# Performance work log

Measured on AMD Instinct MI355X. Metric: run time of the kernel, lower is better.

## Reference

```python
import jax, jax.numpy as jnp
import numpy as np

B = 50000      # batch of graphs
NOBJ = 7       # tangram pieces per graph
HID = 64
EMB = 32
SIGMA = 25.0   # VE-SDE sigma for marginal_prob_std


def _lin_init(k, fin, fout):
    kw, kb = jax.random.split(k)
    s = 1.0 / np.sqrt(fin)
    w = jax.random.uniform(kw, (fin, fout), minval=-s, maxval=s, dtype=jnp.float32)
    b = jax.random.uniform(kb, (fout,), minval=-s, maxval=s, dtype=jnp.float32)
    return w, b


def setup_inputs() -> dict:
    key = jax.random.key(0)
    ks = jax.random.split(key, 16)
    N = B * NOBJ
    omega = jax.random.normal(ks[0], (N, 3), dtype=jnp.float32)
    t = jax.random.uniform(ks[1], (B, 1), minval=1e-3, maxval=1.0, dtype=jnp.float32)
    # fully-connected edges (no self loops) per graph, offset by graph index
    a, b = np.meshgrid(np.arange(NOBJ), np.arange(NOBJ), indexing='ij')
    m = a != b
    src0, dst0 = a[m], b[m]                       # (42,)
    offs = (np.arange(B) * NOBJ)[:, None]         # (B,1)
    src = (src0[None, :] + offs).reshape(-1)
    dst = (dst0[None, :] + offs).reshape(-1)
    edge_index = jnp.asarray(np.stack([src, dst]), dtype=jnp.int32)  # (2, B*42)
    W_fourier = jax.random.normal(ks[2], (EMB // 2,), dtype=jnp.float32) * 30.0
    wi1, bi1 = _lin_init(ks[3], 3, HID)
    wi2, bi2 = _lin_init(ks[4], HID, HID)
    wt, bt = _lin_init(ks[5], EMB, EMB)
    w1a, b1a = _lin_init(ks[6], HID * 2, HID)
    w1b, b1b = _lin_init(ks[7], HID, HID)
    w2a, b2a = _lin_init(ks[8], (HID + EMB) * 2, HID)
    w2b, b2b = _lin_init(ks[9], HID, HID)
    w3a, b3a = _lin_init(ks[10], (HID + EMB) * 2, HID)
    w3b, b3b = _lin_init(ks[11], HID, 3)
    return dict(omega=omega, edge_index=edge_index, t=t, num_objs=NOBJ,
                W_fourier=W_fourier,
                wi1=wi1, bi1=bi1, wi2=wi2, bi2=bi2, wt=wt, bt=bt,
                w1a=w1a, b1a=b1a, w1b=w1b, b1b=b1b,
                w2a=w2a, b2a=b2a, w2b=w2b, b2b=b2b,
                w3a=w3a, b3a=b3a, w3b=w3b, b3b=b3b)


def _mlp(x, wa, ba, wb, bb):
    return jax.nn.relu(x @ wa + ba) @ wb + bb


def reference(omega, edge_index, t, num_objs, W_fourier,
              wi1, bi1, wi2, bi2, wt, bt,
              w1a, b1a, w1b, b1b, w2a, b2a, w2b, b2b, w3a, b3a, w3b, b3b):
    N = omega.shape[0]
    src, dst = edge_index[0], edge_index[1]

    def edge_conv(x, wa, ba, wb, bb):
        # EdgeConv: msg = mlp([x_i, x_j - x_i]); max-aggregate at target i
        xi = x[dst]
        msg = _mlp(jnp.concatenate([xi, x[src] - xi], axis=-1), wa, ba, wb, bb)
        return jax.ops.segment_max(msg, dst, num_segments=N)

    init_feature = _mlp(omega, wi1, bi1, wi2, bi2)          # (N, HID)
    # Gaussian Fourier time embedding -> ReLU -> Linear -> ReLU
    proj = t[:, 0][:, None] * W_fourier[None, :] * (2.0 * jnp.pi)   # (B, EMB/2)
    emb = jnp.concatenate([jnp.sin(proj), jnp.cos(proj)], axis=-1)  # (B, EMB)
    xs = jax.nn.relu(jax.nn.relu(emb) @ wt + bt)                    # (B, EMB)
    # torch: xs.repeat(1, num_objs, 1).view(B*num_objs, -1) == tile whole block
    x_sigma = jnp.tile(xs, (num_objs, 1))                           # (N, EMB)

    x = jax.nn.relu(edge_conv(init_feature, w1a, b1a, w1b, b1b))
    x = jnp.concatenate([x, x_sigma], axis=-1)
    x = jax.nn.relu(edge_conv(x, w2a, b2a, w2b, b2b))
    x = jnp.concatenate([x, x_sigma], axis=-1)
    x = edge_conv(x, w3a, b3a, w3b, b3b)                            # (N, 3)

    # torch: t.repeat(1, num_objs).view(B*num_objs, -1) == repeat_interleave
    t_r = jnp.repeat(t, num_objs, axis=0)                           # (N, 1)
    std = jnp.sqrt((SIGMA ** (2.0 * t_r) - 1.0) / (2.0 * jnp.log(SIGMA)))
    return x / (std + 1e-7)
```

## Files before the change

### kernel.cpp

```cpp
#include <hip/hip_runtime.h>


#define NB 50000

typedef unsigned short u16;
typedef unsigned int u32;
typedef short short8 __attribute__((ext_vector_type(8)));
typedef float f32x4 __attribute__((ext_vector_type(4)));

#define OFF_I  0
#define OFF_1A 8192
#define OFF_2A 24576
#define OFF_3A 49152
#define OFF_1B 73728
#define OFF_2B 81920
#define OFF_WT 90112
#define OFF_3B 92160

#define HSTR 144
#define HLO  2304
#define H2S  272
#define XS2S 72
#define XS2LO 1152
#define SSTR 264
#define WREG 15744

__device__ __forceinline__ float b2f(u16 u) {
    return __uint_as_float(((u32)u) << 16);
}
__device__ __forceinline__ u16 f2b(float f) {
    u32 u = __float_as_uint(f);
    u += 0x7FFFu + ((u >> 16) & 1u);
    return (u16)(u >> 16);
}
__device__ __forceinline__ void split2(float v, u16& h, u16& l) {
    u32 u = __float_as_uint(v);
    h = (u16)(u >> 16);
    float d = v - __uint_as_float(u & 0xffff0000u);
    l = f2b(d);
}
__device__ __forceinline__ u32 splitpack(float v) {
    u32 u = __float_as_uint(v);
    float d = v - __uint_as_float(u & 0xffff0000u);
    u32 r = __float_as_uint(d);
    r += 0x7FFFu + ((r >> 16) & 1u);
    return __builtin_amdgcn_perm(r, u, 0x07060302);
}
__device__ __forceinline__ float bcast(float v, int l) {
    return __uint_as_float(__builtin_amdgcn_readlane(__float_as_uint(v), l));
}

__global__ __launch_bounds__(128) void pack_kernel(
    const float* __restrict__ wi2, const float* __restrict__ w1a,
    const float* __restrict__ w2a, const float* __restrict__ w3a,
    const float* __restrict__ w1b, const float* __restrict__ w2b,
    const float* __restrict__ wt,  const float* __restrict__ w3b,
    u16* __restrict__ ws)
{
    int blk = blockIdx.x;
    int j    = blockIdx.y;
    int half = threadIdx.x >> 6;
    int lane = threadIdx.x & 63;
    float v;
    u16* dst;
    if (blk < 88) {
        const float* src; int NT, qoff, obase, frag;
        if (blk < 8)       { src = wi2; NT = 4; qoff = 0;  obase = OFF_I;  frag = blk;      }
        else if (blk < 24) { src = w1a; NT = 8; qoff = 64; obase = OFF_1A; frag = blk - 8;  }
        else if (blk < 48) { src = w2a; NT = 8; qoff = 96; obase = OFF_2A; frag = blk - 24; }
        else if (blk < 72) { src = w3a; NT = 8; qoff = 96; obase = OFF_3A; frag = blk - 48; }
        else if (blk < 80) { src = w1b; NT = 4; qoff = 0;  obase = OFF_1B; frag = blk - 72; }
        else               { src = w2b; NT = 4; qoff = 0;  obase = OFF_2B; frag = blk - 80; }
        int kt = frag / NT, nt = frag % NT;
        int k = kt * 32 + (lane >> 4) * 8 + j;
        int n = nt * 16 + (lane & 15);
        int idx = (n < 64) ? (k * 64 + n) : ((qoff + k) * 64 + (n - 64));
        v = src[idx];
        dst = ws + obase + frag * 1024 + half * 512 + lane * 8 + j;
    } else if (blk < 90) {
        int frag = blk - 88;
        int k = (lane >> 4) * 8 + j;
        int n = frag * 16 + (lane & 15);
        v = wt[k * 32 + n];
        dst = ws + OFF_WT + frag * 1024 + half * 512 + lane * 8 + j;
    } else {
        int frag = blk - 90;
        int k = frag * 32 + (lane >> 4) * 8 + j;
        int n = lane & 15;
        v = (n < 3) ? w3b[k * 3 + n] : 0.f;
        dst = ws + OFF_3B + frag * 1024 + half * 512 + lane * 8 + j;
    }
    u16 hi = f2b(v);
    *dst = (half == 0) ? hi : f2b(v - b2f(hi));
}

__device__ __forceinline__ f32x4 mfma1(short8 a, short8 b, f32x4 acc) {
    return __builtin_amdgcn_mfma_f32_16x16x32_bf16(a, b, acc, 0, 0, 0);
}
__device__ __forceinline__ f32x4 mfma3(short8 ah, short8 al, short8 bh, short8 bl, f32x4 acc) {
    acc = mfma1(ah, bh, acc);
    acc = mfma1(ah, bl, acc);
    acc = mfma1(al, bh, acc);
    return acc;
}

#define ROW(k) ((k) < 7 ? (k) : (k) + 1)

__device__ __forceinline__ void writeX64_14(char* G, int L, const float* v) {
#pragma unroll
    for (int k = 0; k < 14; ++k) {
        int r = ROW(k);
        u16 h, l;
        split2(v[k], h, l);
        *(u16*)(G + r * HSTR + L * 2) = h;
        *(u16*)(G + HLO + r * HSTR + L * 2) = l;
    }
}
template<int KT>
__device__ __forceinline__ void loadA(const char* G, const char* XS2, int L,
                                      short8* Ah, short8* Al) {
#pragma unroll
    for (int kt = 0; kt < KT; ++kt) {
        if (kt < 2) {
            Ah[kt] = *(const short8*)(G + (L & 15) * HSTR + kt * 64 + (L >> 4) * 16);
            Al[kt] = *(const short8*)(G + HLO + (L & 15) * HSTR + kt * 64 + (L >> 4) * 16);
        } else {
            Ah[kt] = *(const short8*)(XS2 + (L & 15) * XS2S + (L >> 4) * 16);
            Al[kt] = *(const short8*)(XS2 + XS2LO + (L & 15) * XS2S + (L >> 4) * 16);
        }
    }
}
template<int KT, int NT>
__device__ __forceinline__ void lin_pass(const u16* __restrict__ ws, int off, int nt0,
                                         const short8* Ah, const short8* Al,
                                         char* Sg, int L) {
#pragma unroll
    for (int ntc = 0; ntc < 4; ++ntc) {
        f32x4 a1 = {0.f, 0.f, 0.f, 0.f}, a2 = {0.f, 0.f, 0.f, 0.f};
#pragma unroll
        for (int kt = 0; kt < KT; ++kt) {
            int f = kt * NT + nt0 + ntc;
            short8 bh = *(const short8*)(ws + off + f * 1024 + L * 8);
            short8 bl = *(const short8*)(ws + off + f * 1024 + 512 + L * 8);
            a1 = mfma1(Ah[kt], bh, a1);
            a2 = mfma1(Ah[kt], bl, a2);
            a2 = mfma1(Al[kt], bh, a2);
        }
#pragma unroll
        for (int rr = 0; rr < 4; ++rr)
            *(float*)(Sg + ((L >> 4) * 4 + rr) * SSTR + ntc * 64 + (L & 15) * 4) = a1[rr] + a2[rr];
    }
}
__device__ __forceinline__ void readS14(const char* Sg, int L, float* o) {
#pragma unroll
    for (int k = 0; k < 14; ++k) o[k] = *(const float*)(Sg + ROW(k) * SSTR + L * 4);
}
__device__ __forceinline__ void stageH2(char* G, int c, const float* pp, const float* qq, int L) {
#pragma unroll
    for (int r = 0; r < 16; ++r) {
        int e = c * 16 + r;
        if (e < 84) {
            int gb = (e >= 42) ? 1 : 0;
            int el = e - gb * 42;
            int i = el / 6, jj = el - i * 6;
            int j = jj + (jj >= i);
            float hv = fmaxf(pp[gb * 7 + i] + qq[gb * 7 + j], 0.f);
            *(u32*)(G + r * H2S + L * 4) = splitpack(hv);
        }
    }
}
__device__ __forceinline__ void unpack4(const uint4& a, u32* ho, u32* lo) {
    ho[0] = __builtin_amdgcn_perm(a.y, a.x, 0x05040100);
    ho[1] = __builtin_amdgcn_perm(a.w, a.z, 0x05040100);
    lo[0] = __builtin_amdgcn_perm(a.y, a.x, 0x07060302);
    lo[1] = __builtin_amdgcn_perm(a.w, a.z, 0x07060302);
}
__device__ __forceinline__ void loadAH(const char* G, int L,
                                       short8& Ah0, short8& Ah1, short8& Al0, short8& Al1) {
    const char* base = G + (L & 15) * H2S + (L >> 4) * 32;
    uint4 a0 = *(const uint4*)(base);
    uint4 a1 = *(const uint4*)(base + 16);
    uint4 b0 = *(const uint4*)(base + 128);
    uint4 b1 = *(const uint4*)(base + 144);
    union { u32 u[4]; short8 s; } h0, h1, l0, l1;
    unpack4(a0, &h0.u[0], &l0.u[0]);
    unpack4(a1, &h0.u[2], &l0.u[2]);
    unpack4(b0, &h1.u[0], &l1.u[0]);
    unpack4(b1, &h1.u[2], &l1.u[2]);
    Ah0 = h0.s; Al0 = l0.s; Ah1 = h1.s; Al1 = l1.s;
}
__device__ __forceinline__ void maxread(const char* Sb, int cc, float* mx, int L) {
#pragma unroll
    for (int r = 0; r < 16; ++r) {
        int e = cc * 16 + r;
        if (e < 84) {
            int gb = (e >= 42) ? 1 : 0;
            int i = (e - gb * 42) / 6;
            float sv = *(const float*)(Sb + r * SSTR + L * 4);
            mx[gb * 7 + i] = fmaxf(mx[gb * 7 + i], sv);
        }
    }
}

__device__ __forceinline__ void edgeconv_pipe(const u16* __restrict__ ws, int offB,
                                              char* W, char* H1, char* Sb,
                                              const float* pp, const float* qq,
                                              float vb, int L) {
    short8 Bh[8], Bl[8];
#pragma unroll
    for (int f = 0; f < 8; ++f) {
        Bh[f] = *(const short8*)(ws + offB + f * 1024 + L * 8);
        Bl[f] = *(const short8*)(ws + offB + f * 1024 + 512 + L * 8);
    }
    float mx[14];
#pragma unroll
    for (int k = 0; k < 14; ++k) mx[k] = -3.0e38f;
    stageH2(W, 0, pp, qq, L);
    short8 Ah0, Ah1, Al0, Al1;
    loadAH(W, L, Ah0, Ah1, Al0, Al1);
#pragma unroll
    for (int c = 0; c < 6; ++c) {
        char* Hn = ((c + 1) & 1) ? H1 : W;
        if (c < 5) stageH2(Hn, c + 1, pp, qq, L);
        if (c > 0) maxread(Sb, c - 1, mx, L);
#pragma unroll
        for (int nt = 0; nt < 4; ++nt) {
            f32x4 a1 = {0.f, 0.f, 0.f, 0.f}, a2 = {0.f, 0.f, 0.f, 0.f};
            a1 = mfma1(Ah0, Bh[nt], a1);
            a2 = mfma1(Ah0, Bl[nt], a2);
            a2 = mfma1(Al0, Bh[nt], a2);
            a1 = mfma1(Ah1, Bh[4 + nt], a1);
            a2 = mfma1(Ah1, Bl[4 + nt], a2);
            a2 = mfma1(Al1, Bh[4 + nt], a2);
#pragma unroll
            for (int rr = 0; rr < 4; ++rr)
                *(float*)(Sb + ((L >> 4) * 4 + rr) * SSTR + nt * 64 + (L & 15) * 4) = a1[rr] + a2[rr];
        }
        if (c < 5) loadAH(Hn, L, Ah0, Ah1, Al0, Al1);
    }
    maxread(Sb, 5, mx, L);
    float xo[14];
#pragma unroll
    for (int k = 0; k < 14; ++k) xo[k] = fmaxf(mx[k] + vb, 0.f);
    writeX64_14(W, L, xo);
}

__global__ __launch_bounds__(128) void gnn_kernel(
    const float* __restrict__ omega, const float* __restrict__ tt, const float* __restrict__ Wf,
    const float* __restrict__ wi1, const float* __restrict__ bi1, const float* __restrict__ bi2,
    const float* __restrict__ bt,
    const float* __restrict__ b1a, const float* __restrict__ b1b,
    const float* __restrict__ b2a, const float* __restrict__ b2b,
    const float* __restrict__ b3a, const float* __restrict__ b3b,
    const u16* __restrict__ ws, float* __restrict__ out)
{
    __shared__ __align__(16) char smem[2 * WREG];
    const int L   = threadIdx.x & 63;
    const int wav = threadIdx.x >> 6;
    const int p   = blockIdx.x * 2 + wav;
    const int g0  = p * 2;
    const int base0 = g0 * 7;
    char* W   = smem + wav * WREG;
    char* XS2 = W + 4608;
    char* H1  = W + 6912;
    char* Sb  = W + 11520;

    float omv = (L < 42) ? omega[base0 * 3 + L] : 0.f;
    float vwi10 = wi1[L], vwi11 = wi1[64 + L], vwi12 = wi1[128 + L];
    float vbi1 = bi1[L];
    float h1[14];
#pragma unroll
    for (int k = 0; k < 14; ++k) {
        float a0 = bcast(omv, 3 * k), a1 = bcast(omv, 3 * k + 1), a2 = bcast(omv, 3 * k + 2);
        h1[k] = fmaxf(fmaf(a0, vwi10, fmaf(a1, vwi11, fmaf(a2, vwi12, vbi1))), 0.f);
    }

    {
        int cc = L & 31;
        float vwf = Wf[cc & 15] * 6.283185307179586f;
        int tb = base0 - (base0 / NB) * NB;
#pragma unroll
        for (int k = 0; k < 14; ++k) {
            int ti = tb + k; if (ti >= NB) ti -= NB;
            float pj = tt[ti] * vwf;
            float remb = fmaxf((cc < 16) ? __sinf(pj) : __cosf(pj), 0.f);
            u16 h, l;
            split2(remb, h, l);
            if (L < 32) *(u16*)(W + ROW(k) * HSTR + cc * 2) = h;
            else *(u16*)(W + HLO + ROW(k) * HSTR + cc * 2) = l;
        }
        short8 Eh = *(const short8*)(W + (L & 15) * HSTR + (L >> 4) * 16);
        short8 El = *(const short8*)(W + HLO + (L & 15) * HSTR + (L >> 4) * 16);
#pragma unroll
        for (int nt = 0; nt < 2; ++nt) {
            short8 bh = *(const short8*)(ws + OFF_WT + nt * 1024 + L * 8);
            short8 bl = *(const short8*)(ws + OFF_WT + nt * 1024 + 512 + L * 8);
            f32x4 acc = {0.f, 0.f, 0.f, 0.f};
            acc = mfma3(Eh, El, bh, bl, acc);
#pragma unroll
            for (int rr = 0; rr < 4; ++rr)
                *(float*)(Sb + ((L >> 4) * 4 + rr) * SSTR + nt * 64 + (L & 15) * 4) = acc[rr];
        }
        float vbt = bt[cc];
#pragma unroll
        for (int k = 0; k < 14; ++k) {
            float xv = fmaxf(*(const float*)(Sb + ROW(k) * SSTR + cc * 4) + vbt, 0.f);
            u16 h, l;
            split2(xv, h, l);
            if (L < 32) *(u16*)(XS2 + ROW(k) * XS2S + cc * 2) = h;
            else *(u16*)(XS2 + XS2LO + ROW(k) * XS2S + cc * 2) = l;
        }
    }

    short8 Ah[3], Al[3];
    float pp[14], qq[14];

    writeX64_14(W, L, h1);
    loadA<2>(W, XS2, L, Ah, Al);
    lin_pass<2, 4>(ws, OFF_I, 0, Ah, Al, Sb, L);
    {
        float xh[14];
        readS14(Sb, L, xh);
        float vbi2 = bi2[L];
#pragma unroll
        for (int k = 0; k < 14; ++k) xh[k] += vbi2;
        writeX64_14(W, L, xh);
    }

    loadA<2>(W, XS2, L, Ah, Al);
    lin_pass<2, 8>(ws, OFF_1A, 0, Ah, Al, Sb, L);
    readS14(Sb, L, pp);
    lin_pass<2, 8>(ws, OFF_1A, 4, Ah, Al, Sb, L);
    readS14(Sb, L, qq);
    float vb1a = b1a[L];
#pragma unroll
    for (int k = 0; k < 14; ++k) pp[k] = pp[k] + vb1a - qq[k];
    edgeconv_pipe(ws, OFF_1B, W, H1, Sb, pp, qq, b1b[L], L);

    loadA<3>(W, XS2, L, Ah, Al);
    lin_pass<3, 8>(ws, OFF_2A, 0, Ah, Al, Sb, L);
    readS14(Sb, L, pp);
    lin_pass<3, 8>(ws, OFF_2A, 4, Ah, Al, Sb, L);
    readS14(Sb, L, qq);
    float vb2a = b2a[L];
#pragma unroll
    for (int k = 0; k < 14; ++k) pp[k] = pp[k] + vb2a - qq[k];
    edgeconv_pipe(ws, OFF_2B, W, H1, Sb, pp, qq, b2b[L], L);

    loadA<3>(W, XS2, L, Ah, Al);
    lin_pass<3, 8>(ws, OFF_3A, 0, Ah, Al, Sb, L);
    readS14(Sb, L, pp);
    lin_pass<3, 8>(ws, OFF_3A, 4, Ah, Al, Sb, L);
    readS14(Sb, L, qq);
    float vb3a = b3a[L];
#pragma unroll
    for (int k = 0; k < 14; ++k) pp[k] = pp[k] + vb3a - qq[k];

    {
        short8 B0h = *(const short8*)(ws + OFF_3B + L * 8);
        short8 B0l = *(const short8*)(ws + OFF_3B + 512 + L * 8);
        short8 B1h = *(const short8*)(ws + OFF_3B + 1024 + L * 8);
        short8 B1l = *(const short8*)(ws + OFF_3B + 1536 + L * 8);
        stageH2(W, 0, pp, qq, L);
        short8 Ah0, Ah1, Al0, Al1;
        loadAH(W, L, Ah0, Ah1, Al0, Al1);
#pragma unroll
        for (int c = 0; c < 6; ++c) {
            char* Hn = ((c + 1) & 1) ? H1 : W;
            if (c < 5) stageH2(Hn, c + 1, pp, qq, L);
            f32x4 a1 = {0.f, 0.f, 0.f, 0.f}, a2 = {0.f, 0.f, 0.f, 0.f};
            a1 = mfma1(Ah0, B0h, a1);
            a2 = mfma1(Ah0, B0l, a2);
            a2 = mfma1(Al0, B0h, a2);
            a1 = mfma1(Ah1, B1h, a1);
            a2 = mfma1(Ah1, B1l, a2);
            a2 = mfma1(Al1, B1h, a2);
            if ((L & 15) < 3) {
#pragma unroll
                for (int rr = 0; rr < 4; ++rr)
                    *(float*)(Sb + (c * 16 + (L >> 4) * 4 + rr) * 16 + (L & 15) * 4) = a1[rr] + a2[rr];
            }
            if (c < 5) loadAH(Hn, L, Ah0, Ah1, Al0, Al1);
        }
        if (L < 42) {
            int gb = (L >= 21) ? 1 : 0;
            int ll = L - gb * 21;
            int i = ll / 3, col = ll - i * 3;
            int e0 = gb * 42 + i * 6;
            float m = -3.0e38f;
#pragma unroll
            for (int e6 = 0; e6 < 6; ++e6)
                m = fmaxf(m, *(const float*)(Sb + (e0 + e6) * 16 + col * 4));
            m += b3b[col];
            float tg = tt[g0 + gb];
            float stdv = sqrtf((exp2f(tg * 9.287712379549448f) - 1.0f) * 0.15533740282828987f);
            out[base0 * 3 + L] = m / (stdv + 1e-7f);
        }
    }
}

extern "C" void kernel_launch(void* const* d_in, const int* in_sizes, int n_in,
                              void* d_out, int out_size, void* d_ws, size_t ws_size,
                              hipStream_t stream) {
    const float* omega = (const float*)d_in[0];
    const float* tt  = (const float*)d_in[2];
    const float* Wf  = (const float*)d_in[4];
    const float* wi1 = (const float*)d_in[5];
    const float* bi1 = (const float*)d_in[6];
    const float* wi2 = (const float*)d_in[7];
    const float* bi2 = (const float*)d_in[8];
    const float* wt  = (const float*)d_in[9];
    const float* bt  = (const float*)d_in[10];
    const float* w1a = (const float*)d_in[11];
    const float* b1a = (const float*)d_in[12];
    const float* w1b = (const float*)d_in[13];
    const float* b1b = (const float*)d_in[14];
    const float* w2a = (const float*)d_in[15];
    const float* b2a = (const float*)d_in[16];
    const float* w2b = (const float*)d_in[17];
    const float* b2b = (const float*)d_in[18];
    const float* w3a = (const float*)d_in[19];
    const float* b3a = (const float*)d_in[20];
    const float* w3b = (const float*)d_in[21];
    const float* b3b = (const float*)d_in[22];
    u16* ws = (u16*)d_ws;

    pack_kernel<<<dim3(92, 8), dim3(128), 0, stream>>>(wi2, w1a, w2a, w3a, w1b, w2b, wt, w3b, ws);
    gnn_kernel<<<dim3(12500), dim3(128), 0, stream>>>(
        omega, tt, Wf, wi1, bi1, bi2, bt,
        b1a, b1b, b2a, b2b, b3a, b3b, ws, (float*)d_out);
}
```

Baseline: 416.1 us.

## Shrink per-wave LDS by keeping time-embedding fragments in registers, single-buffer H

Removes the separate XS2 shared-memory region: the time-embedding A fragments are loaded once into registers (Ah2/Al2) and reused for the layer-2 and layer-3 linear passes. The H1 double buffer for edge staging is dropped, so staging writes go straight into W. Per-wave LDS falls from 15744 to 8832 bytes, and launch_bounds asks for 4 blocks per SM, both aimed at higher occupancy. The cost is extra live registers, and a single staging buffer means stageH2 for the next chunk overwrites W while the previous loadAH may still be reading it. Within one wave, program order should make that safe.

```diff
diff --git a/kernel.cpp b/kernel.cpp
--- a/kernel.cpp
+++ b/kernel.cpp
@@ -20,10 +20,8 @@
 #define HSTR 144
 #define HLO  2304
 #define H2S  272
-#define XS2S 72
-#define XS2LO 1152
 #define SSTR 264
-#define WREG 15744
+#define WREG 8832
 
 __device__ __forceinline__ float b2f(u16 u) {
     return __uint_as_float(((u32)u) << 16);
@@ -116,18 +114,11 @@
         *(u16*)(G + HLO + r * HSTR + L * 2) = l;
     }
 }
-template<int KT>
-__device__ __forceinline__ void loadA(const char* G, const char* XS2, int L,
-                                      short8* Ah, short8* Al) {
-#pragma unroll
-    for (int kt = 0; kt < KT; ++kt) {
-        if (kt < 2) {
-            Ah[kt] = *(const short8*)(G + (L & 15) * HSTR + kt * 64 + (L >> 4) * 16);
-            Al[kt] = *(const short8*)(G + HLO + (L & 15) * HSTR + kt * 64 + (L >> 4) * 16);
-        } else {
-            Ah[kt] = *(const short8*)(XS2 + (L & 15) * XS2S + (L >> 4) * 16);
-            Al[kt] = *(const short8*)(XS2 + XS2LO + (L & 15) * XS2S + (L >> 4) * 16);
-        }
+__device__ __forceinline__ void loadA2(const char* G, int L, short8* Ah, short8* Al) {
+#pragma unroll
+    for (int kt = 0; kt < 2; ++kt) {
+        Ah[kt] = *(const short8*)(G + (L & 15) * HSTR + kt * 64 + (L >> 4) * 16);
+        Al[kt] = *(const short8*)(G + HLO + (L & 15) * HSTR + kt * 64 + (L >> 4) * 16);
     }
 }
 template<int KT, int NT>
@@ -203,7 +194,7 @@
 }
 
 __device__ __forceinline__ void edgeconv_pipe(const u16* __restrict__ ws, int offB,
-                                              char* W, char* H1, char* Sb,
+                                              char* W, char* Sb,
                                               const float* pp, const float* qq,
                                               float vb, int L) {
     short8 Bh[8], Bl[8];
@@ -220,8 +211,7 @@
     loadAH(W, L, Ah0, Ah1, Al0, Al1);
 #pragma unroll
     for (int c = 0; c < 6; ++c) {
-        char* Hn = ((c + 1) & 1) ? H1 : W;
-        if (c < 5) stageH2(Hn, c + 1, pp, qq, L);
+        if (c < 5) stageH2(W, c + 1, pp, qq, L);
         if (c > 0) maxread(Sb, c - 1, mx, L);
 #pragma unroll
         for (int nt = 0; nt < 4; ++nt) {
@@ -236,7 +226,7 @@
             for (int rr = 0; rr < 4; ++rr)
                 *(float*)(Sb + ((L >> 4) * 4 + rr) * SSTR + nt * 64 + (L & 15) * 4) = a1[rr] + a2[rr];
         }
-        if (c < 5) loadAH(Hn, L, Ah0, Ah1, Al0, Al1);
+        if (c < 5) loadAH(W, L, Ah0, Ah1, Al0, Al1);
     }
     maxread(Sb, 5, mx, L);
     float xo[14];
@@ -245,7 +235,7 @@
     writeX64_14(W, L, xo);
 }
 
-__global__ __launch_bounds__(128) void gnn_kernel(
+__global__ __launch_bounds__(128, 4) void gnn_kernel(
     const float* __restrict__ omega, const float* __restrict__ tt, const float* __restrict__ Wf,
     const float* __restrict__ wi1, const float* __restrict__ bi1, const float* __restrict__ bi2,
     const float* __restrict__ bt,
@@ -261,9 +251,7 @@
     const int g0  = p * 2;
     const int base0 = g0 * 7;
     char* W   = smem + wav * WREG;
-    char* XS2 = W + 4608;
-    char* H1  = W + 6912;
-    char* Sb  = W + 11520;
+    char* Sb  = W + 4608;
 
     float omv = (L < 42) ? omega[base0 * 3 + L] : 0.f;
     float vwi10 = wi1[L], vwi11 = wi1[64 + L], vwi12 = wi1[128 + L];
@@ -275,6 +263,7 @@
         h1[k] = fmaxf(fmaf(a0, vwi10, fmaf(a1, vwi11, fmaf(a2, vwi12, vbi1))), 0.f);
     }
 
+    short8 Ah2, Al2;
     {
         int cc = L & 31;
         float vwf = Wf[cc & 15] * 6.283185307179586f;
@@ -307,16 +296,18 @@
             float xv = fmaxf(*(const float*)(Sb + ROW(k) * SSTR + cc * 4) + vbt, 0.f);
             u16 h, l;
             split2(xv, h, l);
-            if (L < 32) *(u16*)(XS2 + ROW(k) * XS2S + cc * 2) = h;
-            else *(u16*)(XS2 + XS2LO + ROW(k) * XS2S + cc * 2) = l;
-        }
+            if (L < 32) *(u16*)(W + ROW(k) * HSTR + cc * 2) = h;
+            else *(u16*)(W + HLO + ROW(k) * HSTR + cc * 2) = l;
+        }
+        Ah2 = *(const short8*)(W + (L & 15) * HSTR + (L >> 4) * 16);
+        Al2 = *(const short8*)(W + HLO + (L & 15) * HSTR + (L >> 4) * 16);
     }
 
     short8 Ah[3], Al[3];
     float pp[14], qq[14];
 
     writeX64_14(W, L, h1);
-    loadA<2>(W, XS2, L, Ah, Al);
+    loadA2(W, L, Ah, Al);
     lin_pass<2, 4>(ws, OFF_I, 0, Ah, Al, Sb, L);
     {
         float xh[14];
@@ -327,7 +318,7 @@
         writeX64_14(W, L, xh);
     }
 
-    loadA<2>(W, XS2, L, Ah, Al);
+    loadA2(W, L, Ah, Al);
     lin_pass<2, 8>(ws, OFF_1A, 0, Ah, Al, Sb, L);
     readS14(Sb, L, pp);
     lin_pass<2, 8>(ws, OFF_1A, 4, Ah, Al, Sb, L);
@@ -335,9 +326,10 @@
     float vb1a = b1a[L];
 #pragma unroll
     for (int k = 0; k < 14; ++k) pp[k] = pp[k] + vb1a - qq[k];
-    edgeconv_pipe(ws, OFF_1B, W, H1, Sb, pp, qq, b1b[L], L);
-
-    loadA<3>(W, XS2, L, Ah, Al);
+    edgeconv_pipe(ws, OFF_1B, W, Sb, pp, qq, b1b[L], L);
+
+    loadA2(W, L, Ah, Al);
+    Ah[2] = Ah2; Al[2] = Al2;
     lin_pass<3, 8>(ws, OFF_2A, 0, Ah, Al, Sb, L);
     readS14(Sb, L, pp);
     lin_pass<3, 8>(ws, OFF_2A, 4, Ah, Al, Sb, L);
@@ -345,9 +337,10 @@
     float vb2a = b2a[L];
 #pragma unroll
     for (int k = 0; k < 14; ++k) pp[k] = pp[k] + vb2a - qq[k];
-    edgeconv_pipe(ws, OFF_2B, W, H1, Sb, pp, qq, b2b[L], L);
-
-    loadA<3>(W, XS2, L, Ah, Al);
+    edgeconv_pipe(ws, OFF_2B, W, Sb, pp, qq, b2b[L], L);
+
+    loadA2(W, L, Ah, Al);
+    Ah[2] = Ah2; Al[2] = Al2;
     lin_pass<3, 8>(ws, OFF_3A, 0, Ah, Al, Sb, L);
     readS14(Sb, L, pp);
     lin_pass<3, 8>(ws, OFF_3A, 4, Ah, Al, Sb, L);
@@ -366,8 +359,7 @@
         loadAH(W, L, Ah0, Ah1, Al0, Al1);
 #pragma unroll
         for (int c = 0; c < 6; ++c) {
-            char* Hn = ((c + 1) & 1) ? H1 : W;
-            if (c < 5) stageH2(Hn, c + 1, pp, qq, L);
+            if (c < 5) stageH2(W, c + 1, pp, qq, L);
             f32x4 a1 = {0.f, 0.f, 0.f, 0.f}, a2 = {0.f, 0.f, 0.f, 0.f};
             a1 = mfma1(Ah0, B0h, a1);
             a2 = mfma1(Ah0, B0l, a2);
@@ -380,7 +372,7 @@
                 for (int rr = 0; rr < 4; ++rr)
                     *(float*)(Sb + (c * 16 + (L >> 4) * 4 + rr) * 16 + (L & 15) * 4) = a1[rr] + a2[rr];
             }
-            if (c < 5) loadAH(Hn, L, Ah0, Ah1, Al0, Al1);
+            if (c < 5) loadAH(W, L, Ah0, Ah1, Al0, Al1);
         }
         if (L < 42) {
             int gb = (L >= 21) ? 1 : 0;
```

Result: slower. 681.1 us (+63.7%).
